# Kernel optimization log

Measured on AMD Instinct MI355X. Metric: run time of the kernel, lower is better.

Reference implementation:

```python
import jax, jax.numpy as jnp
import numpy as np


def setup_inputs() -> dict:
    key = jax.random.key(0)
    ks = jax.random.split(key, 8)
    dim, E = 128, 8
    b, t, h, w = 2, 16, 64, 64
    scale = 1.0 / np.sqrt(dim)
    return {
        "x": jax.random.normal(ks[0], (b, dim, t, h, w), jnp.float32),
        "gate_w": jax.random.normal(ks[1], (dim, E), jnp.float32) * scale,
        "gate_b": jax.random.normal(ks[2], (E,), jnp.float32) * 0.01,
        "W1": jax.random.normal(ks[3], (E, dim, dim), jnp.float32) * scale,
        "b1": jax.random.normal(ks[4], (E, dim), jnp.float32) * 0.01,
        "alpha": jnp.full((E,), 0.25, jnp.float32),  # PReLU default init
        "W2": jax.random.normal(ks[5], (E, dim, dim), jnp.float32) * scale,
        "b2": jax.random.normal(ks[6], (E, dim), jnp.float32) * 0.01,
        "top_k": 2,
    }


def reference(x, gate_w, gate_b, W1, b1, alpha, W2, b2, top_k):
    b, c, t, h, w = x.shape
    E = gate_w.shape[1]
    # tokens: [N, c] with N = b*t*h*w (matches permute(0,2,3,4,1).reshape(-1,c))
    xf = jnp.transpose(x, (0, 2, 3, 4, 1)).reshape(-1, c)
    N = xf.shape[0]
    logits = xf @ gate_w + gate_b                      # [N, E]
    vals, idx = jax.lax.top_k(logits, top_k)           # [N, K]
    probs = jax.nn.softmax(vals, axis=1)               # softmax over selected logits
    # scatter combine weights to dense [N, E] (zero for unselected experts)
    combine = jnp.zeros((N, E), xf.dtype).at[jnp.arange(N)[:, None], idx].add(probs)
    # expert MLP (1x1x1 conv == per-token linear), scalar PReLU per expert
    h1 = jnp.einsum('nc,eoc->eno', xf, W1) + b1[:, None, :]          # [E, N, c]
    h1 = jnp.maximum(h1, 0) + alpha[:, None, None] * jnp.minimum(h1, 0)
    h2 = jnp.einsum('eno,epo->enp', h1, W2) + b2[:, None, :]         # [E, N, c]
    out = jnp.einsum('ne,enc->nc', combine, h2)                      # weighted combine
    out = jnp.transpose(out.reshape(b, t, h, w, c), (0, 4, 1, 2, 3))
    return out + x
```

## Files before the change

kernel.cpp:

```cpp
#include <hip/hip_runtime.h>

typedef float f32x4 __attribute__((ext_vector_type(4)));
typedef __bf16 bf16x8 __attribute__((ext_vector_type(8)));

#define SPAT 65536
#define CH   128
#define NE   8

#define XS_OFF   0
#define WA_OFF   65536
#define WB_OFF   98304
#define PL_OFF   131072
#define SEL_OFF  139264
#define Q_OFF    140288
#define B1_OFF   142336
#define CB_OFF   146432
#define B2T_OFF  150528
#define AL_OFF   152576
#define LDS_BYTES 152608

static __device__ __forceinline__ unsigned short f2b(float f) {
    unsigned u = __builtin_bit_cast(unsigned, f);
    unsigned r = u + 0x7FFFu + ((u >> 16) & 1u);
    return (unsigned short)(r >> 16);
}
static __device__ __forceinline__ unsigned pk2(float a, float b) {
    return (unsigned)f2b(a) | ((unsigned)f2b(b) << 16);
}

typedef const __attribute__((address_space(1))) void* as1cp;
typedef __attribute__((address_space(3))) void* as3p;
static __device__ __forceinline__ void gload16(const void* g, void* l) {
    __builtin_amdgcn_global_load_lds((as1cp)g, (as3p)l, 16, 0, 0);
}

__global__ void conv_w(const float* __restrict__ W1, const float* __restrict__ W2,
                       unsigned char* __restrict__ wimg) {
    const int gid = blockIdx.x * 256 + threadIdx.x;
    const int mat = gid >> 14;
    const int e   = (gid >> 11) & 7;
    const int o   = (gid >> 4) & 127;
    const int g   = gid & 15;
    const float* s = (mat ? W2 : W1) + (e * 16384 + o * 128 + g * 8);
    uint4 p;
    p.x = pk2(s[0], s[1]); p.y = pk2(s[2], s[3]);
    p.z = pk2(s[4], s[5]); p.w = pk2(s[6], s[7]);
    *(uint4*)(wimg + mat * 262144 + e * 32768 + o * 256 + ((g ^ (o & 7)) * 16)) = p;
}

__global__ __launch_bounds__(512, 2)
void moe_main(const float* __restrict__ x,  const float* __restrict__ gw,
              const float* __restrict__ gb, const float* __restrict__ b1,
              const float* __restrict__ alpha, const float* __restrict__ b2,
              const unsigned char* __restrict__ wimg, float* __restrict__ out)
{
    __shared__ __align__(16) unsigned char smem[LDS_BYTES];
    const int t = threadIdx.x, lane = t & 63, w = t >> 6, blk = blockIdx.x;
    const size_t xbase = (size_t)(blk >> 8) * (size_t)(CH * SPAT) + (size_t)((blk & 255) << 8);

    {
        const int off = w * 1024 + lane * 16, lofs = w * 1024;
        #pragma unroll
        for (int r = 0; r < 4; ++r) {
            gload16(wimg + r * 8192 + off,           smem + WA_OFF + r * 8192 + lofs);
            gload16(wimg + 262144 + r * 8192 + off,  smem + WB_OFF + r * 8192 + lofs);
        }
    }

    if (t < 256) ((f32x4*)(smem + B1_OFF))[t] = ((const f32x4*)b1)[t];
    if (t < 128) {
        uint4 p;
        p.x = pk2(b2[0 * 128 + t], b2[1 * 128 + t]);
        p.y = pk2(b2[2 * 128 + t], b2[3 * 128 + t]);
        p.z = pk2(b2[4 * 128 + t], b2[5 * 128 + t]);
        p.w = pk2(b2[6 * 128 + t], b2[7 * 128 + t]);
        *(uint4*)(smem + B2T_OFF + t * 16) = p;
    }
    if (t < 8) ((float*)(smem + AL_OFF))[t] = alpha[t];

    {
        const int m = t & 255, half = t >> 8;
        f32x4 plo = {0.f,0.f,0.f,0.f}, phi = {0.f,0.f,0.f,0.f};
        #pragma unroll
        for (int cc = 0; cc < 8; ++cc) {
            const int c0 = half * 64 + cc * 8;
            float v[8];
            #pragma unroll
            for (int j = 0; j < 8; ++j) v[j] = x[xbase + (size_t)(c0 + j) * SPAT + m];
            #pragma unroll
            for (int j = 0; j < 8; ++j) {
                const f32x4 g0 = *(const f32x4*)(gw + (c0 + j) * NE);
                const f32x4 g1 = *(const f32x4*)(gw + (c0 + j) * NE + 4);
                plo += v[j] * g0; phi += v[j] * g1;
            }
            uint4 pkv;
            pkv.x = pk2(v[0], v[1]); pkv.y = pk2(v[2], v[3]);
            pkv.z = pk2(v[4], v[5]); pkv.w = pk2(v[6], v[7]);
            const int g = half * 8 + cc;
            *(uint4*)(smem + XS_OFF + m * 256 + ((g ^ (m & 7)) * 16)) = pkv;
        }
        if (half) {
            *(f32x4*)(smem + PL_OFF + m * 32)      = plo;
            *(f32x4*)(smem + PL_OFF + m * 32 + 16) = phi;
        }
        __syncthreads();
        if (!half) {
            const f32x4 rlo = *(const f32x4*)(smem + PL_OFF + m * 32);
            const f32x4 rhi = *(const f32x4*)(smem + PL_OFF + m * 32 + 16);
            float lg[8];
            #pragma unroll
            for (int e2 = 0; e2 < 4; ++e2) {
                lg[e2]     = plo[e2] + rlo[e2] + gb[e2];
                lg[4 + e2] = phi[e2] + rhi[e2] + gb[4 + e2];
            }
            int i0 = 0; float v0 = lg[0];
            #pragma unroll
            for (int e2 = 1; e2 < 8; ++e2) if (lg[e2] > v0) { v0 = lg[e2]; i0 = e2; }
            int i1 = -1; float v1 = -3.4e38f;
            #pragma unroll
            for (int e2 = 0; e2 < 8; ++e2) if (e2 != i0 && lg[e2] > v1) { v1 = lg[e2]; i1 = e2; }
            const float d  = expf(v1 - v0);
            const float q0 = 1.f / (1.f + d);
            const float q1 = d   / (1.f + d);
            ((unsigned*)(smem + SEL_OFF))[m] = (unsigned)i0 | ((unsigned)i1 << 8);
            ((float*)(smem + Q_OFF))[m * 2]     = q0;
            ((float*)(smem + Q_OFF))[m * 2 + 1] = q1;
            float cb[8];
            #pragma unroll
            for (int e2 = 0; e2 < 8; ++e2)
                cb[e2] = (e2 == i0) ? q0 : ((e2 == i1) ? q1 : 0.f);
            uint4 cw;
            cw.x = pk2(cb[0], cb[1]); cw.y = pk2(cb[2], cb[3]);
            cw.z = pk2(cb[4], cb[5]); cw.w = pk2(cb[6], cb[7]);
            *(uint4*)(smem + CB_OFF + m * 16) = cw;
        }
    }
    __syncthreads();

    const int mg = w >> 2, ng = w & 3, col = lane & 15, kq = lane >> 4;

    int sel[4]; float cp0[4], cp1[4];
    #pragma unroll
    for (int nf = 0; nf < 4; ++nf) {
        const int tk = ng * 64 + nf * 16 + col;
        sel[nf] = ((const unsigned*)(smem + SEL_OFF))[tk];
        cp0[nf] = ((const float*)(smem + Q_OFF))[tk * 2];
        cp1[nf] = ((const float*)(smem + Q_OFF))[tk * 2 + 1];
    }
    uint4 xb[4][4];
    #pragma unroll
    for (int nf = 0; nf < 4; ++nf) {
        const int row = ng * 64 + nf * 16 + col;
        #pragma unroll
        for (int kt = 0; kt < 4; ++kt)
            xb[nf][kt] = *(const uint4*)(smem + XS_OFF + row * 256 + (((kt * 4 + kq) ^ (row & 7)) * 16));
    }
    __syncthreads();

    f32x4 acc[4][4] = {};

    for (int e = 0; e < NE; ++e) {
        const float alph = ((const float*)(smem + AL_OFF))[e];
        #pragma unroll
        for (int ml = 0; ml < 4; ++ml) {
            const int mt = mg * 4 + ml;
            const int o  = mt * 16 + col;
            uint4 a1[4];
            #pragma unroll
            for (int kt = 0; kt < 4; ++kt)
                a1[kt] = *(const uint4*)(smem + WA_OFF + o * 256 + (((kt * 4 + kq) ^ (o & 7)) * 16));
            f32x4 h[4] = {};
            #pragma unroll
            for (int kt = 0; kt < 4; ++kt)
                #pragma unroll
                for (int nf = 0; nf < 4; ++nf)
                    h[nf] = __builtin_amdgcn_mfma_f32_16x16x32_bf16(
                        __builtin_bit_cast(bf16x8, a1[kt]),
                        __builtin_bit_cast(bf16x8, xb[nf][kt]), h[nf], 0, 0, 0);
            const f32x4 b1v = *(const f32x4*)(smem + B1_OFF + e * 512 + (mt * 16 + kq * 4) * 4);
            #pragma unroll
            for (int nf = 0; nf < 4; ++nf) {
                const float ce = ((sel[nf] & 255) == e) ? cp0[nf]
                               : ((((sel[nf] >> 8) & 255) == e) ? cp1[nf] : 0.f);
                float hv[4];
                #pragma unroll
                for (int i = 0; i < 4; ++i) {
                    float z = h[nf][i] + b1v[i];
                    z = (z > 0.f) ? z : alph * z;
                    hv[i] = z * ce;
                }
                const int tok = ng * 64 + nf * 16 + col;
                const int o0  = mt * 16 + kq * 4;
                const int g   = o0 >> 3;
                uint2 pw; pw.x = pk2(hv[0], hv[1]); pw.y = pk2(hv[2], hv[3]);
                *(uint2*)(smem + XS_OFF + tok * 256 + ((g ^ (tok & 7)) * 16) + ((o0 & 4) << 1)) = pw;
            }
        }
        __syncthreads();
        if (e < 7) {
            const int off = w * 1024 + lane * 16, lofs = w * 1024;
            const unsigned char* src = wimg + (e + 1) * 32768;
            #pragma unroll
            for (int r = 0; r < 4; ++r)
                gload16(src + r * 8192 + off, smem + WA_OFF + r * 8192 + lofs);
        }
        #pragma unroll
        for (int kt = 0; kt < 4; ++kt) {
            uint4 hb[4], wf[4];
            #pragma unroll
            for (int m2 = 0; m2 < 4; ++m2) {
                const int tok = ng * 64 + m2 * 16 + col;
                hb[m2] = *(const uint4*)(smem + XS_OFF + tok * 256 + (((kt * 4 + kq) ^ (tok & 7)) * 16));
            }
            #pragma unroll
            for (int n2 = 0; n2 < 4; ++n2) {
                const int o2 = mg * 64 + n2 * 16 + col;
                wf[n2] = *(const uint4*)(smem + WB_OFF + o2 * 256 + (((kt * 4 + kq) ^ (o2 & 7)) * 16));
            }
            #pragma unroll
            for (int m2 = 0; m2 < 4; ++m2)
                #pragma unroll
                for (int n2 = 0; n2 < 4; ++n2)
                    acc[m2][n2] = __builtin_amdgcn_mfma_f32_16x16x32_bf16(
                        __builtin_bit_cast(bf16x8, hb[m2]),
                        __builtin_bit_cast(bf16x8, wf[n2]), acc[m2][n2], 0, 0, 0);
        }
        __syncthreads();
        if (e < 7) {
            const int off = w * 1024 + lane * 16, lofs = w * 1024;
            const unsigned char* src = wimg + 262144 + (e + 1) * 32768;
            #pragma unroll
            for (int r = 0; r < 4; ++r)
                gload16(src + r * 8192 + off, smem + WB_OFF + r * 8192 + lofs);
        }
    }

    {
        const uint4 z4 = {0u, 0u, 0u, 0u};
        uint4 paf[4], pbf[4];
        #pragma unroll
        for (int m2 = 0; m2 < 4; ++m2) {
            const int tok = ng * 64 + m2 * 16 + col;
            paf[m2] = (kq == 0) ? *(const uint4*)(smem + CB_OFF + tok * 16) : z4;
        }
        #pragma unroll
        for (int n2 = 0; n2 < 4; ++n2) {
            const int o2 = mg * 64 + n2 * 16 + col;
            pbf[n2] = (kq == 0) ? *(const uint4*)(smem + B2T_OFF + o2 * 16) : z4;
        }
        #pragma unroll
        for (int m2 = 0; m2 < 4; ++m2)
            #pragma unroll
            for (int n2 = 0; n2 < 4; ++n2)
                acc[m2][n2] = __builtin_amdgcn_mfma_f32_16x16x32_bf16(
                    __builtin_bit_cast(bf16x8, paf[m2]),
                    __builtin_bit_cast(bf16x8, pbf[n2]), acc[m2][n2], 0, 0, 0);
    }

    #pragma unroll
    for (int m2 = 0; m2 < 4; ++m2) {
        const int tok0 = ng * 64 + m2 * 16 + kq * 4;
        #pragma unroll
        for (int n2 = 0; n2 < 4; ++n2) {
            const int o2 = mg * 64 + n2 * 16 + col;
            const size_t a = xbase + (size_t)o2 * SPAT + tok0;
            const f32x4 xv = *(const f32x4*)(x + a);
            f32x4 r = acc[m2][n2];
            r += xv;
            *(f32x4*)(out + a) = r;
        }
    }
}

extern "C" void kernel_launch(void* const* d_in, const int* in_sizes, int n_in,
                              void* d_out, int out_size, void* d_ws, size_t ws_size,
                              hipStream_t stream) {
    const float* x  = (const float*)d_in[0];
    const float* gw = (const float*)d_in[1];
    const float* gb = (const float*)d_in[2];
    const float* W1 = (const float*)d_in[3];
    const float* b1 = (const float*)d_in[4];
    const float* al = (const float*)d_in[5];
    const float* W2 = (const float*)d_in[6];
    const float* b2 = (const float*)d_in[7];
    (void)in_sizes; (void)n_in; (void)out_size; (void)ws_size;
    unsigned char* wimg = (unsigned char*)d_ws;
    float* out = (float*)d_out;

    conv_w<<<dim3(128), dim3(256), 0, stream>>>(W1, W2, wimg);
    moe_main<<<dim3(512), dim3(512), 0, stream>>>(x, gw, gb, b1, al, b2, wimg, out);
}
```

Measured before the change: 128.5 us.

## Double block size to 16 waves with halved per-wave token tiles and aliased LDS

Launches 1024-thread blocks instead of 512, so each wave owns 32 tokens rather than 64 in both expert GEMMs. The gating partial-logit reduction is spread over four thread groups. The partial-logit buffer now aliases the W1 staging area, which shrinks the LDS footprint, so the initial weight prefetch is moved to after routing is finished. The aim is more resident waves per CU to hide memory and MFMA latency, at the cost of more redundant LDS weight-fragment reads per MFMA and losing the overlap of the first weight load with the x load.

```diff
diff --git a/kernel.cpp b/kernel.cpp
--- a/kernel.cpp
+++ b/kernel.cpp
@@ -10,14 +10,14 @@
 #define XS_OFF   0
 #define WA_OFF   65536
 #define WB_OFF   98304
-#define PL_OFF   131072
-#define SEL_OFF  139264
-#define Q_OFF    140288
-#define B1_OFF   142336
-#define CB_OFF   146432
-#define B2T_OFF  150528
-#define AL_OFF   152576
-#define LDS_BYTES 152608
+#define PL_OFF   65536
+#define SEL_OFF  131072
+#define Q_OFF    132096
+#define CB_OFF   134144
+#define B1_OFF   138240
+#define B2T_OFF  142336
+#define AL_OFF   144384
+#define LDS_BYTES 144416
 
 static __device__ __forceinline__ unsigned short f2b(float f) {
     unsigned u = __builtin_bit_cast(unsigned, f);
@@ -48,7 +48,7 @@
     *(uint4*)(wimg + mat * 262144 + e * 32768 + o * 256 + ((g ^ (o & 7)) * 16)) = p;
 }
 
-__global__ __launch_bounds__(512, 2)
+__global__ __launch_bounds__(1024, 4)
 void moe_main(const float* __restrict__ x,  const float* __restrict__ gw,
               const float* __restrict__ gb, const float* __restrict__ b1,
               const float* __restrict__ alpha, const float* __restrict__ b2,
@@ -58,32 +58,25 @@
     const int t = threadIdx.x, lane = t & 63, w = t >> 6, blk = blockIdx.x;
     const size_t xbase = (size_t)(blk >> 8) * (size_t)(CH * SPAT) + (size_t)((blk & 255) << 8);
 
+    if (t < 256) ((f32x4*)(smem + B1_OFF))[t] = ((const f32x4*)b1)[t];
+    else if (t >= 256 && t < 384) {
+        const int j = t - 256;
+        uint4 p;
+        p.x = pk2(b2[0 * 128 + j], b2[1 * 128 + j]);
+        p.y = pk2(b2[2 * 128 + j], b2[3 * 128 + j]);
+        p.z = pk2(b2[4 * 128 + j], b2[5 * 128 + j]);
+        p.w = pk2(b2[6 * 128 + j], b2[7 * 128 + j]);
+        *(uint4*)(smem + B2T_OFF + j * 16) = p;
+    } else if (t >= 384 && t < 392) {
+        ((float*)(smem + AL_OFF))[t - 384] = alpha[t - 384];
+    }
+
     {
-        const int off = w * 1024 + lane * 16, lofs = w * 1024;
-        #pragma unroll
-        for (int r = 0; r < 4; ++r) {
-            gload16(wimg + r * 8192 + off,           smem + WA_OFF + r * 8192 + lofs);
-            gload16(wimg + 262144 + r * 8192 + off,  smem + WB_OFF + r * 8192 + lofs);
-        }
-    }
-
-    if (t < 256) ((f32x4*)(smem + B1_OFF))[t] = ((const f32x4*)b1)[t];
-    if (t < 128) {
-        uint4 p;
-        p.x = pk2(b2[0 * 128 + t], b2[1 * 128 + t]);
-        p.y = pk2(b2[2 * 128 + t], b2[3 * 128 + t]);
-        p.z = pk2(b2[4 * 128 + t], b2[5 * 128 + t]);
-        p.w = pk2(b2[6 * 128 + t], b2[7 * 128 + t]);
-        *(uint4*)(smem + B2T_OFF + t * 16) = p;
-    }
-    if (t < 8) ((float*)(smem + AL_OFF))[t] = alpha[t];
-
-    {
-        const int m = t & 255, half = t >> 8;
+        const int m = t & 255, p = t >> 8;
         f32x4 plo = {0.f,0.f,0.f,0.f}, phi = {0.f,0.f,0.f,0.f};
         #pragma unroll
-        for (int cc = 0; cc < 8; ++cc) {
-            const int c0 = half * 64 + cc * 8;
+        for (int cc = 0; cc < 4; ++cc) {
+            const int c0 = p * 32 + cc * 8;
             float v[8];
             #pragma unroll
             for (int j = 0; j < 8; ++j) v[j] = x[xbase + (size_t)(c0 + j) * SPAT + m];
@@ -96,90 +89,101 @@
             uint4 pkv;
             pkv.x = pk2(v[0], v[1]); pkv.y = pk2(v[2], v[3]);
             pkv.z = pk2(v[4], v[5]); pkv.w = pk2(v[6], v[7]);
-            const int g = half * 8 + cc;
+            const int g = p * 4 + cc;
             *(uint4*)(smem + XS_OFF + m * 256 + ((g ^ (m & 7)) * 16)) = pkv;
         }
-        if (half) {
-            *(f32x4*)(smem + PL_OFF + m * 32)      = plo;
-            *(f32x4*)(smem + PL_OFF + m * 32 + 16) = phi;
-        }
-        __syncthreads();
-        if (!half) {
-            const f32x4 rlo = *(const f32x4*)(smem + PL_OFF + m * 32);
-            const f32x4 rhi = *(const f32x4*)(smem + PL_OFF + m * 32 + 16);
-            float lg[8];
-            #pragma unroll
-            for (int e2 = 0; e2 < 4; ++e2) {
-                lg[e2]     = plo[e2] + rlo[e2] + gb[e2];
-                lg[4 + e2] = phi[e2] + rhi[e2] + gb[4 + e2];
-            }
-            int i0 = 0; float v0 = lg[0];
-            #pragma unroll
-            for (int e2 = 1; e2 < 8; ++e2) if (lg[e2] > v0) { v0 = lg[e2]; i0 = e2; }
-            int i1 = -1; float v1 = -3.4e38f;
-            #pragma unroll
-            for (int e2 = 0; e2 < 8; ++e2) if (e2 != i0 && lg[e2] > v1) { v1 = lg[e2]; i1 = e2; }
-            const float d  = expf(v1 - v0);
-            const float q0 = 1.f / (1.f + d);
-            const float q1 = d   / (1.f + d);
-            ((unsigned*)(smem + SEL_OFF))[m] = (unsigned)i0 | ((unsigned)i1 << 8);
-            ((float*)(smem + Q_OFF))[m * 2]     = q0;
-            ((float*)(smem + Q_OFF))[m * 2 + 1] = q1;
-            float cb[8];
-            #pragma unroll
-            for (int e2 = 0; e2 < 8; ++e2)
-                cb[e2] = (e2 == i0) ? q0 : ((e2 == i1) ? q1 : 0.f);
-            uint4 cw;
-            cw.x = pk2(cb[0], cb[1]); cw.y = pk2(cb[2], cb[3]);
-            cw.z = pk2(cb[4], cb[5]); cw.w = pk2(cb[6], cb[7]);
-            *(uint4*)(smem + CB_OFF + m * 16) = cw;
+        float* pl = (float*)(smem + PL_OFF);
+        #pragma unroll
+        for (int e2 = 0; e2 < 4; ++e2) {
+            pl[(p * 8 + e2)     * 256 + m] = plo[e2];
+            pl[(p * 8 + 4 + e2) * 256 + m] = phi[e2];
         }
     }
     __syncthreads();
-
-    const int mg = w >> 2, ng = w & 3, col = lane & 15, kq = lane >> 4;
-
-    int sel[4]; float cp0[4], cp1[4];
+    if (t < 256) {
+        const int m = t;
+        const float* pl = (const float*)(smem + PL_OFF);
+        float lg[8];
+        #pragma unroll
+        for (int e2 = 0; e2 < 8; ++e2) lg[e2] = gb[e2];
+        #pragma unroll
+        for (int pp = 0; pp < 4; ++pp)
+            #pragma unroll
+            for (int e2 = 0; e2 < 8; ++e2) lg[e2] += pl[(pp * 8 + e2) * 256 + m];
+        int i0 = 0; float v0 = lg[0];
+        #pragma unroll
+        for (int e2 = 1; e2 < 8; ++e2) if (lg[e2] > v0) { v0 = lg[e2]; i0 = e2; }
+        int i1 = -1; float v1 = -3.4e38f;
+        #pragma unroll
+        for (int e2 = 0; e2 < 8; ++e2) if (e2 != i0 && lg[e2] > v1) { v1 = lg[e2]; i1 = e2; }
+        const float d  = expf(v1 - v0);
+        const float q0 = 1.f / (1.f + d);
+        const float q1 = d   / (1.f + d);
+        ((unsigned*)(smem + SEL_OFF))[m] = (unsigned)i0 | ((unsigned)i1 << 8);
+        ((float*)(smem + Q_OFF))[m * 2]     = q0;
+        ((float*)(smem + Q_OFF))[m * 2 + 1] = q1;
+        float cb[8];
+        #pragma unroll
+        for (int e2 = 0; e2 < 8; ++e2) cb[e2] = (e2 == i0) ? q0 : ((e2 == i1) ? q1 : 0.f);
+        uint4 cw;
+        cw.x = pk2(cb[0], cb[1]); cw.y = pk2(cb[2], cb[3]);
+        cw.z = pk2(cb[4], cb[5]); cw.w = pk2(cb[6], cb[7]);
+        *(uint4*)(smem + CB_OFF + m * 16) = cw;
+    }
+    __syncthreads();
+
+    {
+        const int goff = w * 1024 + lane * 16, loff = w * 1024;
+        #pragma unroll
+        for (int r = 0; r < 2; ++r) {
+            gload16(wimg + r * 16384 + goff,          smem + WA_OFF + r * 16384 + loff);
+            gload16(wimg + 262144 + r * 16384 + goff, smem + WB_OFF + r * 16384 + loff);
+        }
+    }
+
+    const int mg = w >> 3, ng = w & 7, col = lane & 15, kq = lane >> 4;
+
+    int sel[2]; float cp0[2], cp1[2];
     #pragma unroll
-    for (int nf = 0; nf < 4; ++nf) {
-        const int tk = ng * 64 + nf * 16 + col;
+    for (int nf = 0; nf < 2; ++nf) {
+        const int tk = ng * 32 + nf * 16 + col;
         sel[nf] = ((const unsigned*)(smem + SEL_OFF))[tk];
         cp0[nf] = ((const float*)(smem + Q_OFF))[tk * 2];
         cp1[nf] = ((const float*)(smem + Q_OFF))[tk * 2 + 1];
     }
-    uint4 xb[4][4];
+    uint4 xb[2][4];
     #pragma unroll
-    for (int nf = 0; nf < 4; ++nf) {
-        const int row = ng * 64 + nf * 16 + col;
+    for (int nf = 0; nf < 2; ++nf) {
+        const int row = ng * 32 + nf * 16 + col;
         #pragma unroll
         for (int kt = 0; kt < 4; ++kt)
             xb[nf][kt] = *(const uint4*)(smem + XS_OFF + row * 256 + (((kt * 4 + kq) ^ (row & 7)) * 16));
     }
     __syncthreads();
 
-    f32x4 acc[4][4] = {};
+    f32x4 acc[2][4] = {};
 
     for (int e = 0; e < NE; ++e) {
         const float alph = ((const float*)(smem + AL_OFF))[e];
         #pragma unroll
         for (int ml = 0; ml < 4; ++ml) {
-            const int mt = mg * 4 + ml;
-            const int o  = mt * 16 + col;
+            const int o = mg * 64 + ml * 16 + col;
             uint4 a1[4];
             #pragma unroll
             for (int kt = 0; kt < 4; ++kt)
                 a1[kt] = *(const uint4*)(smem + WA_OFF + o * 256 + (((kt * 4 + kq) ^ (o & 7)) * 16));
-            f32x4 h[4] = {};
+            f32x4 h[2] = {};
             #pragma unroll
             for (int kt = 0; kt < 4; ++kt)
                 #pragma unroll
-                for (int nf = 0; nf < 4; ++nf)
+                for (int nf = 0; nf < 2; ++nf)
                     h[nf] = __builtin_amdgcn_mfma_f32_16x16x32_bf16(
                         __builtin_bit_cast(bf16x8, a1[kt]),
                         __builtin_bit_cast(bf16x8, xb[nf][kt]), h[nf], 0, 0, 0);
-            const f32x4 b1v = *(const f32x4*)(smem + B1_OFF + e * 512 + (mt * 16 + kq * 4) * 4);
-            #pragma unroll
-            for (int nf = 0; nf < 4; ++nf) {
+            const int o0 = mg * 64 + ml * 16 + kq * 4;
+            const f32x4 b1v = *(const f32x4*)(smem + B1_OFF + e * 512 + o0 * 4);
+            #pragma unroll
+            for (int nf = 0; nf < 2; ++nf) {
                 const float ce = ((sel[nf] & 255) == e) ? cp0[nf]
                                : ((((sel[nf] >> 8) & 255) == e) ? cp1[nf] : 0.f);
                 float hv[4];
@@ -189,8 +193,7 @@
                     z = (z > 0.f) ? z : alph * z;
                     hv[i] = z * ce;
                 }
-                const int tok = ng * 64 + nf * 16 + col;
-                const int o0  = mt * 16 + kq * 4;
+                const int tok = ng * 32 + nf * 16 + col;
                 const int g   = o0 >> 3;
                 uint2 pw; pw.x = pk2(hv[0], hv[1]); pw.y = pk2(hv[2], hv[3]);
                 *(uint2*)(smem + XS_OFF + tok * 256 + ((g ^ (tok & 7)) * 16) + ((o0 & 4) << 1)) = pw;
@@ -198,18 +201,18 @@
         }
         __syncthreads();
         if (e < 7) {
-            const int off = w * 1024 + lane * 16, lofs = w * 1024;
+            const int goff = w * 1024 + lane * 16, loff = w * 1024;
             const unsigned char* src = wimg + (e + 1) * 32768;
             #pragma unroll
-            for (int r = 0; r < 4; ++r)
-                gload16(src + r * 8192 + off, smem + WA_OFF + r * 8192 + lofs);
+            for (int r = 0; r < 2; ++r)
+                gload16(src + r * 16384 + goff, smem + WA_OFF + r * 16384 + loff);
         }
         #pragma unroll
         for (int kt = 0; kt < 4; ++kt) {
-            uint4 hb[4], wf[4];
-            #pragma unroll
-            for (int m2 = 0; m2 < 4; ++m2) {
-                const int tok = ng * 64 + m2 * 16 + col;
+            uint4 hb[2], wf[4];
+            #pragma unroll
+            for (int m2 = 0; m2 < 2; ++m2) {
+                const int tok = ng * 32 + m2 * 16 + col;
                 hb[m2] = *(const uint4*)(smem + XS_OFF + tok * 256 + (((kt * 4 + kq) ^ (tok & 7)) * 16));
             }
             #pragma unroll
@@ -218,7 +221,7 @@
                 wf[n2] = *(const uint4*)(smem + WB_OFF + o2 * 256 + (((kt * 4 + kq) ^ (o2 & 7)) * 16));
             }
             #pragma unroll
-            for (int m2 = 0; m2 < 4; ++m2)
+            for (int m2 = 0; m2 < 2; ++m2)
                 #pragma unroll
                 for (int n2 = 0; n2 < 4; ++n2)
                     acc[m2][n2] = __builtin_amdgcn_mfma_f32_16x16x32_bf16(
@@ -227,20 +230,20 @@
         }
         __syncthreads();
         if (e < 7) {
-            const int off = w * 1024 + lane * 16, lofs = w * 1024;
+            const int goff = w * 1024 + lane * 16, loff = w * 1024;
             const unsigned char* src = wimg + 262144 + (e + 1) * 32768;
             #pragma unroll
-            for (int r = 0; r < 4; ++r)
-                gload16(src + r * 8192 + off, smem + WB_OFF + r * 8192 + lofs);
+            for (int r = 0; r < 2; ++r)
+                gload16(src + r * 16384 + goff, smem + WB_OFF + r * 16384 + loff);
         }
     }
 
     {
         const uint4 z4 = {0u, 0u, 0u, 0u};
-        uint4 paf[4], pbf[4];
-        #pragma unroll
-        for (int m2 = 0; m2 < 4; ++m2) {
-            const int tok = ng * 64 + m2 * 16 + col;
+        uint4 paf[2], pbf[4];
+        #pragma unroll
+        for (int m2 = 0; m2 < 2; ++m2) {
+            const int tok = ng * 32 + m2 * 16 + col;
             paf[m2] = (kq == 0) ? *(const uint4*)(smem + CB_OFF + tok * 16) : z4;
         }
         #pragma unroll
@@ -249,7 +252,7 @@
             pbf[n2] = (kq == 0) ? *(const uint4*)(smem + B2T_OFF + o2 * 16) : z4;
         }
         #pragma unroll
-        for (int m2 = 0; m2 < 4; ++m2)
+        for (int m2 = 0; m2 < 2; ++m2)
             #pragma unroll
             for (int n2 = 0; n2 < 4; ++n2)
                 acc[m2][n2] = __builtin_amdgcn_mfma_f32_16x16x32_bf16(
@@ -258,8 +261,8 @@
     }
 
     #pragma unroll
-    for (int m2 = 0; m2 < 4; ++m2) {
-        const int tok0 = ng * 64 + m2 * 16 + kq * 4;
+    for (int m2 = 0; m2 < 2; ++m2) {
+        const int tok0 = ng * 32 + m2 * 16 + kq * 4;
         #pragma unroll
         for (int n2 = 0; n2 < 4; ++n2) {
             const int o2 = mg * 64 + n2 * 16 + col;
@@ -288,5 +291,5 @@
     float* out = (float*)d_out;
 
     conv_w<<<dim3(128), dim3(256), 0, stream>>>(W1, W2, wimg);
-    moe_main<<<dim3(512), dim3(512), 0, stream>>>(x, gw, gb, b1, al, b2, wimg, out);
-}
+    moe_main<<<dim3(512), dim3(1024), 0, stream>>>(x, gw, gb, b1, al, b2, wimg, out);
+}
```

New measurement: 145.0 us. 1.13x slower.
